# Optimization experiments

Measured on AMD Instinct MI355X. Metric: run time of the kernel, lower is better.

Reference implementation:

```python
import jax, jax.numpy as jnp
import numpy as np

N = 50000      # nodes
E = 800000     # edges
H = 128        # hidden_dim
EF = 16        # edge_feat_dim
EIN = 2 * H + 1 + EF  # edge MLP input dim = 273


def setup_inputs() -> dict:
    key = jax.random.key(0)
    ks = jax.random.split(key, 20)
    s = 0.05
    return {
        "h": jax.random.normal(ks[0], (N, H), jnp.float32),
        "x": jax.random.normal(ks[1], (N, 3), jnp.float32),
        "edge_attr": jax.random.normal(ks[2], (E, EF), jnp.float32),
        # edge MLP: Linear(EIN,H) -> SiLU -> Linear(H,H) -> SiLU
        "we_w1": jax.random.normal(ks[3], (EIN, H), jnp.float32) * s,
        "we_b1": jnp.zeros((H,), jnp.float32),
        "we_w2": jax.random.normal(ks[4], (H, H), jnp.float32) * s,
        "we_b2": jnp.zeros((H,), jnp.float32),
        # coord MLP: Linear(H,H) -> SiLU -> Linear(H,1, bias=False), tiny init
        "wc_w1": jax.random.normal(ks[5], (H, H), jnp.float32) * s,
        "wc_b1": jnp.zeros((H,), jnp.float32),
        "wc_w2": jax.random.normal(ks[6], (H, 1), jnp.float32) * 0.001,
        # node MLP: Linear(2H,H) -> SiLU -> Linear(H,H)
        "wn_w1": jax.random.normal(ks[7], (2 * H, H), jnp.float32) * s,
        "wn_b1": jnp.zeros((H,), jnp.float32),
        "wn_w2": jax.random.normal(ks[8], (H, H), jnp.float32) * s,
        "wn_b2": jnp.zeros((H,), jnp.float32),
        # layer norm
        "ln_g": jnp.ones((H,), jnp.float32),
        "ln_b": jnp.zeros((H,), jnp.float32),
        "edge_index": jax.random.randint(ks[9], (2, E), 0, N, dtype=jnp.int32),
    }


def reference(h, x, edge_attr, we_w1, we_b1, we_w2, we_b2,
              wc_w1, wc_b1, wc_w2, wn_w1, wn_b1, wn_w2, wn_b2,
              ln_g, ln_b, edge_index):
    row, col = edge_index[0], edge_index[1]
    n = h.shape[0]

    coord_diff = x[row] - x[col]                         # [E, 3]
    dist_sq = jnp.sum(coord_diff ** 2, axis=-1, keepdims=True)  # [E, 1]

    edge_input = jnp.concatenate([h[row], h[col], dist_sq, edge_attr], axis=-1)  # [E, EIN]
    m_ij = jax.nn.silu(edge_input @ we_w1 + we_b1)
    m_ij = jax.nn.silu(m_ij @ we_w2 + we_b2)             # [E, H]

    # coordinate update
    coord_w = jnp.tanh(jax.nn.silu(m_ij @ wc_w1 + wc_b1) @ wc_w2)  # [E, 1]
    dist = jnp.sqrt(dist_sq + 1e-8)
    weighted_diff = (coord_diff / dist) * coord_w        # [E, 3]
    x_update = jax.ops.segment_sum(weighted_diff, row, num_segments=n)
    degree = jax.ops.segment_sum(jnp.ones((row.shape[0], 1), x.dtype), row, num_segments=n)
    degree = jnp.maximum(degree, 1.0)
    x_out = x + x_update / degree

    # node update with residual + layernorm
    m_i = jax.ops.segment_sum(m_ij, row, num_segments=n)  # [N, H]
    node_input = jnp.concatenate([h, m_i], axis=-1)       # [N, 2H]
    h_res = h + (jax.nn.silu(node_input @ wn_w1 + wn_b1) @ wn_w2 + wn_b2)

    mu = jnp.mean(h_res, axis=-1, keepdims=True)
    var = jnp.var(h_res, axis=-1, keepdims=True)
    h_out = (h_res - mu) * jax.lax.rsqrt(var + 1e-5) * ln_g + ln_b
    return (h_out, x_out)
```

## Files before the change

kernel.cpp:

```cpp
#include <hip/hip_runtime.h>

typedef unsigned short u16;
typedef unsigned int u32;
using short8 = __attribute__((ext_vector_type(8))) short;
using f32x4  = __attribute__((ext_vector_type(4))) float;
using u32x4  = __attribute__((ext_vector_type(4))) u32;

#define N_CNT 50000
#define E_CNT 800000
#define EB_CNT 400000

__device__ __forceinline__ u16 f2bf(float f) {
  u32 u = __builtin_bit_cast(u32, f);
  u += 0x7fffu + ((u >> 16) & 1u);
  return (u16)(u >> 16);
}
__device__ __forceinline__ float bf2f(u16 v) {
  u32 u = ((u32)v) << 16;
  return __builtin_bit_cast(float, u);
}
__device__ __forceinline__ float siluf(float v) {
  return __fdividef(v, 1.f + __expf(-v));
}

__global__ void k_wf(const float* __restrict__ w1, const float* __restrict__ w2,
                     const float* __restrict__ wc1, const float* __restrict__ wn1,
                     const float* __restrict__ wn2,
                     u16* __restrict__ wef, u16* __restrict__ w1abf,
                     u16* __restrict__ wnf) {
  int idx = blockIdx.x * 256 + threadIdx.x;
  int i = idx & 7, l = (idx >> 3) & 63;
  int kb = 8 * (l >> 4) + i;
  int n16 = l & 15;
  if (idx < 4096) {
    int t = idx >> 9;
    int k = kb, n = 16 * t + n16;
    wef[idx] = (k < 17) ? f2bf(w1[(256 + k) * 128 + n]) : (u16)0;
  } else if (idx < 20480) {
    int u = idx - 4096, rest = u >> 9;
    int s = rest & 3, t = rest >> 2;
    wef[idx] = f2bf(w2[(32 * s + kb) * 128 + 16 * t + n16]);
  } else if (idx < 36864) {
    int u = idx - 20480, rest = u >> 9;
    int s = rest & 3, t = rest >> 2;
    wef[idx] = f2bf(wc1[(32 * s + kb) * 128 + 16 * t + n16]);
  } else if (idx < 69632) {
    int u = idx - 36864, rest = u >> 9;
    int s = rest & 3, t = rest >> 2;
    int k = 32 * s + kb, n = 16 * t + n16;
    float v = (n < 128) ? w1[k * 128 + n] : w1[(128 + k) * 128 + (n - 128)];
    w1abf[u] = f2bf(v);
  } else if (idx < 102400) {
    int u = idx - 69632, rest = u >> 9;
    int s = rest & 7, t = rest >> 3;
    wnf[u] = f2bf(wn1[(32 * s + kb) * 128 + 16 * t + n16]);
  } else if (idx < 118784) {
    int u = idx - 102400, rest = u >> 9;
    int s = rest & 3, t = rest >> 2;
    wnf[32768 + u] = f2bf(wn2[(32 * s + kb) * 128 + 16 * t + n16]);
  }
}

__global__ __launch_bounds__(256)
void k_hp(const float* __restrict__ h, const u16* __restrict__ w1abf,
          const float* __restrict__ b1v, u16* __restrict__ hp) {
  extern __shared__ char smem[];
  u16* wl = (u16*)smem;
  const int tid = threadIdx.x;
  {
    const u32x4* src = reinterpret_cast<const u32x4*>(w1abf);
    u32x4* dst = reinterpret_cast<u32x4*>(smem);
    for (int i2 = tid; i2 < 4096; i2 += 256) dst[i2] = src[i2];
  }
  __syncthreads();
  const int w = tid >> 6, lane = tid & 63;
  const int g = lane >> 4, c15 = lane & 15;
  float b1r[8];
#pragma unroll
  for (int t = 0; t < 8; ++t) b1r[t] = b1v[t * 16 + c15];

  int wt = blockIdx.x * 4 + w;
  if (wt >= 3125) return;
  int nbase = wt * 16;
  int nr = nbase + c15;
  short8 af[4];
#pragma unroll
  for (int s = 0; s < 4; ++s) {
    const float* p = h + nr * 128 + s * 32 + g * 8;
    f32x4 v0 = *reinterpret_cast<const f32x4*>(p);
    f32x4 v1 = *reinterpret_cast<const f32x4*>(p + 4);
    short8 t8;
#pragma unroll
    for (int j = 0; j < 4; ++j) t8[j] = (short)f2bf(v0[j]);
#pragma unroll
    for (int j = 0; j < 4; ++j) t8[4 + j] = (short)f2bf(v1[j]);
    af[s] = t8;
  }
  f32x4 acc[16];
#pragma unroll
  for (int t = 0; t < 16; ++t) acc[t] = (f32x4){0.f, 0.f, 0.f, 0.f};
#pragma unroll
  for (int s = 0; s < 4; ++s) {
#pragma unroll
    for (int t = 0; t < 16; ++t) {
      short8 bf = *reinterpret_cast<const short8*>(wl + ((t * 4 + s) * 64 + lane) * 8);
      acc[t] = __builtin_amdgcn_mfma_f32_16x16x32_bf16(af[s], bf, acc[t], 0, 0, 0);
    }
  }
#pragma unroll
  for (int t = 0; t < 16; ++t)
#pragma unroll
    for (int i = 0; i < 4; ++i) {
      int row = nbase + g * 4 + i;
      float v = acc[t][i] + ((t < 8) ? b1r[t] : 0.f);
      hp[row * 256 + t * 16 + c15] = f2bf(v);
    }
}

__global__ void k_deg(const int* __restrict__ eidx, int* __restrict__ degs) {
  int e = blockIdx.x * 256 + threadIdx.x;
  int b = (e >= EB_CNT) ? 1 : 0;
  atomicAdd(&degs[b * N_CNT + eidx[e]], 1);
}

__global__ __launch_bounds__(1024)
void k_scan2(const int* __restrict__ degs, int* __restrict__ rps) {
  const int* deg = degs + blockIdx.x * N_CNT;
  int* rp = rps + blockIdx.x * (N_CNT + 1);
  __shared__ int wsum[16];
  __shared__ int carry_s;
  int tid = threadIdx.x, lane = tid & 63, wv = tid >> 6;
  if (tid == 0) carry_s = 0;
  __syncthreads();
  for (int base = 0; base < 50176; base += 1024) {
    int idx = base + tid;
    int v = (idx < N_CNT) ? deg[idx] : 0;
    int inc = v;
#pragma unroll
    for (int d = 1; d < 64; d <<= 1) {
      int u = __shfl_up(inc, d, 64);
      if (lane >= d) inc += u;
    }
    if (lane == 63) wsum[wv] = inc;
    __syncthreads();
    if (tid < 16) {
      int s = wsum[tid];
#pragma unroll
      for (int d = 1; d < 16; d <<= 1) {
        int u = __shfl_up(s, d, 16);
        if (tid >= d) s += u;
      }
      wsum[tid] = s;
    }
    __syncthreads();
    int carry = carry_s;
    int woff = (wv > 0) ? wsum[wv - 1] : 0;
    if (idx < N_CNT) rp[idx] = carry + woff + inc - v;
    __syncthreads();
    if (tid == 0) carry_s = carry + wsum[15];
    __syncthreads();
  }
  if (threadIdx.x == 0) rp[N_CNT] = EB_CNT;
}

__global__ void k_scatter(const int* __restrict__ eidx, const int* __restrict__ rps,
                          int* __restrict__ curs, int* __restrict__ pos) {
  int e = blockIdx.x * 256 + threadIdx.x;
  int b = (e >= EB_CNT) ? 1 : 0;
  int r = eidx[e];
  int p = atomicAdd(&curs[b * N_CNT + r], 1);
  pos[e] = rps[b * (N_CNT + 1) + r] + p;
}

__global__ __launch_bounds__(1024)
void egnn_edge2(const u16* __restrict__ hp, const float* __restrict__ xc,
                const float* __restrict__ ea, const int* __restrict__ eidx,
                const int* __restrict__ pos, const u16* __restrict__ wef,
                const float* __restrict__ b2v, const float* __restrict__ bc1v,
                const float* __restrict__ wc2v,
                u16* __restrict__ m_ij, float* __restrict__ x_acc, int ebase0) {
  extern __shared__ char smem[];
  const int tid = threadIdx.x;
  {
    const u32x4* src = reinterpret_cast<const u32x4*>(wef);
    u32x4* dst = reinterpret_cast<u32x4*>(smem);
    for (int i2 = tid; i2 < 4608; i2 += 1024) dst[i2] = src[i2];
  }
  __syncthreads();
  const int w = tid >> 6, lane = tid & 63;
  const int g = lane >> 4, c15 = lane & 15;
  const int e4 = lane >> 2, q4 = lane & 3;
  const u16* w1tf = (const u16*)smem;
  const u16* w2f  = (const u16*)(smem + 8192);
  const u16* wc1f = (const u16*)(smem + 40960);
  u16* mbuf = (u16*)(smem + 73728 + w * 4352);

  float b2r[8], bc1r[8], wc2r[8];
#pragma unroll
  for (int t = 0; t < 8; ++t) {
    b2r[t]  = b2v[t * 16 + c15];
    bc1r[t] = bc1v[t * 16 + c15];
    wc2r[t] = wc2v[t * 16 + c15];
  }

  for (int bt = blockIdx.x; bt < 1563; bt += gridDim.x) {
    int wt = bt * 16 + w;
    if (wt >= 25000) continue;
    const int eb = ebase0 + wt * 16;
    int r_v = 0, c_v = 0, p_v = 0;
    if (lane < 16) {
      int gi = eb + lane;
      r_v = eidx[gi]; c_v = eidx[E_CNT + gi]; p_v = pos[gi];
      float d0 = xc[3 * r_v + 0] - xc[3 * c_v + 0];
      float d1 = xc[3 * r_v + 1] - xc[3 * c_v + 1];
      float d2 = xc[3 * r_v + 2] - xc[3 * c_v + 2];
      float dsq = d0 * d0 + d1 * d1 + d2 * d2;
      f32x4 cd = {d0, d1, d2, dsq};
      *reinterpret_cast<f32x4*>(mbuf + lane * 136 + 128) = cd;
    }
    int re4 = __shfl(r_v, e4, 64);
    int ce4 = __shfl(c_v, e4, 64);
    int pc15 = __shfl(p_v, c15, 64);
    short8 ga[4], gb[4];
    {
      const u16* pa = hp + re4 * 256 + q4 * 32;
      const u16* pb = hp + ce4 * 256 + 128 + q4 * 32;
#pragma unroll
      for (int q = 0; q < 4; ++q) ga[q] = *reinterpret_cast<const short8*>(pa + q * 8);
#pragma unroll
      for (int q = 0; q < 4; ++q) gb[q] = *reinterpret_cast<const short8*>(pb + q * 8);
    }
    {
      f32x4 eav = *reinterpret_cast<const f32x4*>(ea + (size_t)(eb + e4) * 16 + q4 * 4);
#pragma unroll
      for (int jj = 0; jj < 4; ++jj)
        mbuf[e4 * 136 + 1 + q4 * 4 + jj] = f2bf(eav[jj]);
      if (q4 == 0) {
        float dq = reinterpret_cast<const float*>(mbuf + e4 * 136 + 128)[3];
        mbuf[e4 * 136] = f2bf(dq);
      }
#pragma unroll
      for (int z = 17 + q4; z < 32; z += 4) mbuf[e4 * 136 + z] = 0;
    }
    short8 af8 = *reinterpret_cast<const short8*>(mbuf + c15 * 136 + g * 8);
    f32x4 acc[8];
#pragma unroll
    for (int t = 0; t < 8; ++t) acc[t] = (f32x4){0.f, 0.f, 0.f, 0.f};
#pragma unroll
    for (int t = 0; t < 8; ++t) {
      short8 bf = *reinterpret_cast<const short8*>(w1tf + (t * 64 + lane) * 8);
      acc[t] = __builtin_amdgcn_mfma_f32_16x16x32_bf16(af8, bf, acc[t], 0, 0, 0);
    }
#pragma unroll
    for (int t = 0; t < 8; ++t)
#pragma unroll
      for (int i = 0; i < 4; ++i)
        mbuf[(g * 4 + i) * 136 + t * 16 + c15] = f2bf(acc[t][i]);
#pragma unroll
    for (int q = 0; q < 4; ++q) {
      short8 tl = *reinterpret_cast<const short8*>(mbuf + e4 * 136 + q4 * 32 + q * 8);
      short8 o;
#pragma unroll
      for (int j = 0; j < 8; ++j) {
        float v = bf2f((u16)tl[j]) + bf2f((u16)ga[q][j]) + bf2f((u16)gb[q][j]);
        o[j] = (short)f2bf(siluf(v));
      }
      *reinterpret_cast<short8*>(mbuf + e4 * 136 + q4 * 32 + q * 8) = o;
    }
    short8 a2[4];
#pragma unroll
    for (int s = 0; s < 4; ++s)
      a2[s] = *reinterpret_cast<const short8*>(mbuf + c15 * 136 + s * 32 + g * 8);
    f32x4 acc2[8];
#pragma unroll
    for (int t = 0; t < 8; ++t) acc2[t] = (f32x4){0.f, 0.f, 0.f, 0.f};
#pragma unroll
    for (int s = 0; s < 4; ++s) {
#pragma unroll
      for (int t = 0; t < 8; ++t) {
        short8 bf = *reinterpret_cast<const short8*>(w2f + ((t * 4 + s) * 64 + lane) * 8);
        acc2[t] = __builtin_amdgcn_mfma_f32_16x16x32_bf16(a2[s], bf, acc2[t], 0, 0, 0);
      }
    }
#pragma unroll
    for (int t = 0; t < 8; ++t)
#pragma unroll
      for (int i = 0; i < 4; ++i) {
        float v = siluf(acc2[t][i] + b2r[t]);
        mbuf[(g * 4 + i) * 136 + t * 16 + c15] = f2bf(v);
      }
    short8 a3[4];
#pragma unroll
    for (int q = 0; q < 4; ++q) {
      a3[q] = *reinterpret_cast<const short8*>(mbuf + c15 * 136 + q * 32 + g * 8);
      *reinterpret_cast<short8*>(m_ij + (size_t)pc15 * 128 + q * 32 + g * 8) = a3[q];
    }
    f32x4 acc3[8];
#pragma unroll
    for (int t = 0; t < 8; ++t) acc3[t] = (f32x4){0.f, 0.f, 0.f, 0.f};
#pragma unroll
    for (int s = 0; s < 4; ++s) {
#pragma unroll
      for (int t = 0; t < 8; ++t) {
        short8 bf = *reinterpret_cast<const short8*>(wc1f + ((t * 4 + s) * 64 + lane) * 8);
        acc3[t] = __builtin_amdgcn_mfma_f32_16x16x32_bf16(a3[s], bf, acc3[t], 0, 0, 0);
      }
    }
    float p4[4] = {0.f, 0.f, 0.f, 0.f};
#pragma unroll
    for (int t = 0; t < 8; ++t)
#pragma unroll
      for (int i = 0; i < 4; ++i)
        p4[i] += siluf(acc3[t][i] + bc1r[t]) * wc2r[t];
#pragma unroll
    for (int m = 1; m <= 8; m <<= 1) {
#pragma unroll
      for (int i = 0; i < 4; ++i) p4[i] += __shfl_xor(p4[i], m, 64);
    }
    int rr[4];
#pragma unroll
    for (int i = 0; i < 4; ++i) rr[i] = __shfl(r_v, g * 4 + i, 64);
    if (c15 == 0) {
#pragma unroll
      for (int i = 0; i < 4; ++i) {
        f32x4 cd = *reinterpret_cast<const f32x4*>(mbuf + (g * 4 + i) * 136 + 128);
        float fac = rsqrtf(cd[3] + 1e-8f) * tanhf(p4[i]);
        atomicAdd(&x_acc[rr[i] * 4 + 0], cd[0] * fac);
        atomicAdd(&x_acc[rr[i] * 4 + 1], cd[1] * fac);
        atomicAdd(&x_acc[rr[i] * 4 + 2], cd[2] * fac);
      }
    }
  }
}

template <int ACC>
__global__ __launch_bounds__(256)
void k_gather(const u16* __restrict__ m_ij, const int* __restrict__ rp,
              float* __restrict__ m_i) {
  const int tid = threadIdx.x, w = tid >> 6, lane = tid & 63;
  const int grp = lane >> 4, c16 = lane & 15;
  int node = blockIdx.x * 4 + w;
  int beg = rp[node], end = rp[node + 1];
  float a[8] = {0.f, 0.f, 0.f, 0.f, 0.f, 0.f, 0.f, 0.f};
  for (int j = beg + grp; j < end; j += 4) {
    short8 v = *reinterpret_cast<const short8*>(m_ij + (size_t)j * 128 + c16 * 8);
#pragma unroll
    for (int k = 0; k < 8; ++k) a[k] += bf2f((u16)v[k]);
  }
#pragma unroll
  for (int k = 0; k < 8; ++k) {
    a[k] += __shfl_xor(a[k], 16, 64);
    a[k] += __shfl_xor(a[k], 32, 64);
  }
  if (grp == 0) {
    float* dst = m_i + node * 128 + c16 * 8;
    if (ACC) {
      f32x4 o0 = *reinterpret_cast<const f32x4*>(dst);
      f32x4 o1 = *reinterpret_cast<const f32x4*>(dst + 4);
#pragma unroll
      for (int k = 0; k < 4; ++k) { o0[k] += a[k]; o1[k] += a[4 + k]; }
      *reinterpret_cast<f32x4*>(dst) = o0;
      *reinterpret_cast<f32x4*>(dst + 4) = o1;
    } else {
      f32x4 o0 = {a[0], a[1], a[2], a[3]};
      f32x4 o1 = {a[4], a[5], a[6], a[7]};
      *reinterpret_cast<f32x4*>(dst) = o0;
      *reinterpret_cast<f32x4*>(dst + 4) = o1;
    }
  }
}

__global__ __launch_bounds__(256)
void egnn_node2(const float* __restrict__ h, const float* __restrict__ m_i,
                const u16* __restrict__ wnf,
                const float* __restrict__ bn1, const float* __restrict__ bn2,
                const float* __restrict__ lng, const float* __restrict__ lnb,
                float* __restrict__ h_out) {
  __shared__ u16 mbuf_all[4][2176];
  const int tid = threadIdx.x, w = tid >> 6, lane = tid & 63;
  const int g = lane >> 4, c15 = lane & 15;
  u16* mbuf = mbuf_all[w];
  const u16* wn1f = wnf;
  const u16* wn2f = wnf + 32768;

  float bn1r[8], bn2r[8], lngr[8], lnbr[8];
#pragma unroll
  for (int t = 0; t < 8; ++t) {
    bn1r[t] = bn1[t * 16 + c15];
    bn2r[t] = bn2[t * 16 + c15];
    lngr[t] = lng[t * 16 + c15];
    lnbr[t] = lnb[t * 16 + c15];
  }

  int wt = blockIdx.x * 4 + w;
  if (wt >= 3125) return;
  int nbase = wt * 16;
  int nr = nbase + c15;
  short8 af[8];
#pragma unroll
  for (int s = 0; s < 4; ++s) {
    const float* p = h + nr * 128 + s * 32 + g * 8;
    f32x4 v0 = *reinterpret_cast<const f32x4*>(p);
    f32x4 v1 = *reinterpret_cast<const f32x4*>(p + 4);
    short8 t8;
#pragma unroll
    for (int j = 0; j < 4; ++j) t8[j] = (short)f2bf(v0[j]);
#pragma unroll
    for (int j = 0; j < 4; ++j) t8[4 + j] = (short)f2bf(v1[j]);
    af[s] = t8;
  }
#pragma unroll
  for (int s = 0; s < 4; ++s) {
    const float* p = m_i + nr * 128 + s * 32 + g * 8;
    f32x4 v0 = *reinterpret_cast<const f32x4*>(p);
    f32x4 v1 = *reinterpret_cast<const f32x4*>(p + 4);
    short8 t8;
#pragma unroll
    for (int j = 0; j < 4; ++j) t8[j] = (short)f2bf(v0[j]);
#pragma unroll
    for (int j = 0; j < 4; ++j) t8[4 + j] = (short)f2bf(v1[j]);
    af[4 + s] = t8;
  }
  f32x4 acc[8];
#pragma unroll
  for (int t = 0; t < 8; ++t) acc[t] = (f32x4){0.f, 0.f, 0.f, 0.f};
#pragma unroll
  for (int s = 0; s < 8; ++s) {
#pragma unroll
    for (int t = 0; t < 8; ++t) {
      short8 bf = *reinterpret_cast<const short8*>(wn1f + ((t * 8 + s) * 64 + lane) * 8);
      acc[t] = __builtin_amdgcn_mfma_f32_16x16x32_bf16(af[s], bf, acc[t], 0, 0, 0);
    }
  }
#pragma unroll
  for (int t = 0; t < 8; ++t)
#pragma unroll
    for (int i = 0; i < 4; ++i) {
      float v = siluf(acc[t][i] + bn1r[t]);
      mbuf[(g * 4 + i) * 136 + t * 16 + c15] = f2bf(v);
    }
  short8 a2[4];
#pragma unroll
  for (int s = 0; s < 4; ++s)
    a2[s] = *reinterpret_cast<const short8*>(mbuf + c15 * 136 + s * 32 + g * 8);
  f32x4 acc2[8];
#pragma unroll
  for (int t = 0; t < 8; ++t) acc2[t] = (f32x4){0.f, 0.f, 0.f, 0.f};
#pragma unroll
  for (int s = 0; s < 4; ++s) {
#pragma unroll
    for (int t = 0; t < 8; ++t) {
      short8 bf = *reinterpret_cast<const short8*>(wn2f + ((t * 4 + s) * 64 + lane) * 8);
      acc2[t] = __builtin_amdgcn_mfma_f32_16x16x32_bf16(a2[s], bf, acc2[t], 0, 0, 0);
    }
  }
  float vres[8][4];
  float s1[4] = {0.f, 0.f, 0.f, 0.f}, s2[4] = {0.f, 0.f, 0.f, 0.f};
#pragma unroll
  for (int t = 0; t < 8; ++t)
#pragma unroll
    for (int i = 0; i < 4; ++i) {
      int n = nbase + g * 4 + i;
      float v = acc2[t][i] + bn2r[t] + h[n * 128 + t * 16 + c15];
      vres[t][i] = v; s1[i] += v; s2[i] += v * v;
    }
#pragma unroll
  for (int m = 1; m <= 8; m <<= 1) {
#pragma unroll
    for (int i = 0; i < 4; ++i) {
      s1[i] += __shfl_xor(s1[i], m, 64);
      s2[i] += __shfl_xor(s2[i], m, 64);
    }
  }
  float mu[4], rstd[4];
#pragma unroll
  for (int i = 0; i < 4; ++i) {
    mu[i] = s1[i] * (1.0f / 128.0f);
    float var = s2[i] * (1.0f / 128.0f) - mu[i] * mu[i];
    rstd[i] = rsqrtf(var + 1e-5f);
  }
#pragma unroll
  for (int t = 0; t < 8; ++t)
#pragma unroll
    for (int i = 0; i < 4; ++i) {
      int n = nbase + g * 4 + i;
      h_out[n * 128 + t * 16 + c15] =
          (vres[t][i] - mu[i]) * rstd[i] * lngr[t] + lnbr[t];
    }
}

__global__ void egnn_xout(const float* __restrict__ x, const float* __restrict__ x_acc,
                          const int* __restrict__ degs, float* __restrict__ xo) {
  int n = blockIdx.x * 256 + threadIdx.x;
  if (n < N_CNT) {
    float dg = fmaxf((float)(degs[n] + degs[N_CNT + n]), 1.0f);
    xo[n * 3 + 0] = x[n * 3 + 0] + x_acc[n * 4 + 0] / dg;
    xo[n * 3 + 1] = x[n * 3 + 1] + x_acc[n * 4 + 1] / dg;
    xo[n * 3 + 2] = x[n * 3 + 2] + x_acc[n * 4 + 2] / dg;
  }
}

extern "C" void kernel_launch(void* const* d_in, const int* in_sizes, int n_in,
                              void* d_out, int out_size, void* d_ws, size_t ws_size,
                              hipStream_t stream) {
  const float* h     = (const float*)d_in[0];
  const float* x     = (const float*)d_in[1];
  const float* ea    = (const float*)d_in[2];
  const float* we_w1 = (const float*)d_in[3];
  const float* we_b1 = (const float*)d_in[4];
  const float* we_w2 = (const float*)d_in[5];
  const float* we_b2 = (const float*)d_in[6];
  const float* wc_w1 = (const float*)d_in[7];
  const float* wc_b1 = (const float*)d_in[8];
  const float* wc_w2 = (const float*)d_in[9];
  const float* wn_w1 = (const float*)d_in[10];
  const float* wn_b1 = (const float*)d_in[11];
  const float* wn_w2 = (const float*)d_in[12];
  const float* wn_b2 = (const float*)d_in[13];
  const float* ln_g  = (const float*)d_in[14];
  const float* ln_b  = (const float*)d_in[15];
  const int* eidx    = (const int*)d_in[16];
  float* out = (float*)d_out;
  char* ws = (char*)d_ws;

  u16* wef    = (u16*)(ws);
  u16* w1abf  = (u16*)(ws + 73728);
  u16* wnf    = (u16*)(ws + 139264);
  u16* hp     = (u16*)(ws + 237568);
  float* m_i  = (float*)(ws + 25837568);
  float* xacc = (float*)(ws + 51437568);
  int* degs   = (int*)(ws + 52237568);
  int* curs   = (int*)(ws + 52637568);
  int* rps    = (int*)(ws + 53037568);
  int* pos    = (int*)(ws + 53437584);
  u16* m_ij   = (u16*)(ws + 56637584);

  k_wf<<<464, 256, 0, stream>>>(we_w1, we_w2, wc_w1, wn_w1, wn_w2, wef, w1abf, wnf);

  hipFuncSetAttribute(reinterpret_cast<const void*>(k_hp),
                      hipFuncAttributeMaxDynamicSharedMemorySize, 65536);
  k_hp<<<782, 256, 65536, stream>>>(h, w1abf, we_b1, hp);

  hipMemsetAsync(ws + 51437568, 0, 1600000, stream);
  k_deg<<<3125, 256, 0, stream>>>(eidx, degs);
  k_scan2<<<2, 1024, 0, stream>>>(degs, rps);
  k_scatter<<<3125, 256, 0, stream>>>(eidx, rps, curs, pos);

  hipFuncSetAttribute(reinterpret_cast<const void*>(egnn_edge2),
                      hipFuncAttributeMaxDynamicSharedMemorySize, 143360);
  egnn_edge2<<<256, 1024, 143360, stream>>>(hp, x, ea, eidx, pos, wef,
                                            we_b2, wc_b1, wc_w2, m_ij, xacc, 0);
  k_gather<0><<<12500, 256, 0, stream>>>(m_ij, rps, m_i);
  egnn_edge2<<<256, 1024, 143360, stream>>>(hp, x, ea, eidx, pos, wef,
                                            we_b2, wc_b1, wc_w2, m_ij, xacc, EB_CNT);
  k_gather<1><<<12500, 256, 0, stream>>>(m_ij, rps + (N_CNT + 1), m_i);

  egnn_node2<<<782, 256, 0, stream>>>(h, m_i, wnf, wn_b1, wn_b2, ln_g, ln_b, out);
  egnn_xout<<<196, 256, 0, stream>>>(x, xacc, degs, out + 6400000);
}
```

Measured before the change: 503.8 us.

## Parallelize row-pointer scan and retile edge kernel for higher occupancy

```diff
diff --git a/kernel.cpp b/kernel.cpp
--- a/kernel.cpp
+++ b/kernel.cpp
@@ -18,6 +18,14 @@
 __device__ __forceinline__ float bf2f(u16 v) {
   u32 u = ((u32)v) << 16;
   return __builtin_bit_cast(float, u);
+}
+__device__ __forceinline__ short8 pack8(f32x4 v0, f32x4 v1) {
+  short8 r;
+#pragma unroll
+  for (int j = 0; j < 4; ++j) r[j] = (short)f2bf(v0[j]);
+#pragma unroll
+  for (int j = 0; j < 4; ++j) r[4 + j] = (short)f2bf(v1[j]);
+  return r;
 }
 __device__ __forceinline__ float siluf(float v) {
   return __fdividef(v, 1.f + __expf(-v));
@@ -87,14 +95,8 @@
 #pragma unroll
   for (int s = 0; s < 4; ++s) {
     const float* p = h + nr * 128 + s * 32 + g * 8;
-    f32x4 v0 = *reinterpret_cast<const f32x4*>(p);
-    f32x4 v1 = *reinterpret_cast<const f32x4*>(p + 4);
-    short8 t8;
-#pragma unroll
-    for (int j = 0; j < 4; ++j) t8[j] = (short)f2bf(v0[j]);
-#pragma unroll
-    for (int j = 0; j < 4; ++j) t8[4 + j] = (short)f2bf(v1[j]);
-    af[s] = t8;
+    af[s] = pack8(*reinterpret_cast<const f32x4*>(p),
+                  *reinterpret_cast<const f32x4*>(p + 4));
   }
   f32x4 acc[16];
 #pragma unroll
@@ -108,13 +110,13 @@
     }
   }
 #pragma unroll
-  for (int t = 0; t < 16; ++t)
-#pragma unroll
-    for (int i = 0; i < 4; ++i) {
-      int row = nbase + g * 4 + i;
-      float v = acc[t][i] + ((t < 8) ? b1r[t] : 0.f);
-      hp[row * 256 + t * 16 + c15] = f2bf(v);
-    }
+  for (int t = 0; t < 16; ++t) {
+    float bb = (t < 8) ? b1r[t] : 0.f;
+    int col = t * 16 + c15;
+#pragma unroll
+    for (int i = 0; i < 4; ++i)
+      hp[(size_t)(nbase + g * 4 + i) * 256 + col] = f2bf(acc[t][i] + bb);
+  }
 }
 
 __global__ void k_deg(const int* __restrict__ eidx, int* __restrict__ degs) {
@@ -123,44 +125,67 @@
   atomicAdd(&degs[b * N_CNT + eidx[e]], 1);
 }
 
-__global__ __launch_bounds__(1024)
-void k_scan2(const int* __restrict__ degs, int* __restrict__ rps) {
-  const int* deg = degs + blockIdx.x * N_CNT;
-  int* rp = rps + blockIdx.x * (N_CNT + 1);
-  __shared__ int wsum[16];
-  __shared__ int carry_s;
-  int tid = threadIdx.x, lane = tid & 63, wv = tid >> 6;
-  if (tid == 0) carry_s = 0;
+__global__ void k_bsum(const int* __restrict__ degs, int* __restrict__ bsum) {
+  int bid = blockIdx.x;
+  int batch = bid / 98, chunk = bid % 98;
+  const int* deg = degs + batch * N_CNT;
+  int b0 = chunk * 512 + threadIdx.x;
+  int b1 = b0 + 256;
+  int v = ((b0 < N_CNT) ? deg[b0] : 0) + ((b1 < N_CNT) ? deg[b1] : 0);
+#pragma unroll
+  for (int m = 1; m <= 32; m <<= 1) v += __shfl_xor(v, m, 64);
+  __shared__ int ws[4];
+  if ((threadIdx.x & 63) == 0) ws[threadIdx.x >> 6] = v;
   __syncthreads();
-  for (int base = 0; base < 50176; base += 1024) {
-    int idx = base + tid;
-    int v = (idx < N_CNT) ? deg[idx] : 0;
+  if (threadIdx.x == 0) bsum[bid] = ws[0] + ws[1] + ws[2] + ws[3];
+}
+
+__global__ void k_mid(const int* __restrict__ bsum, int* __restrict__ boff,
+                      int* __restrict__ rps) {
+  int wv = threadIdx.x >> 6, lane = threadIdx.x & 63;
+  if (wv >= 2) return;
+  const int* bs = bsum + wv * 98;
+  int* bo = boff + wv * 98;
+  int carry = 0;
+  for (int base = 0; base < 98; base += 64) {
+    int idx = base + lane;
+    int v = (idx < 98) ? bs[idx] : 0;
     int inc = v;
 #pragma unroll
-    for (int d = 1; d < 64; d <<= 1) {
+    for (int d = 1; d <= 32; d <<= 1) {
       int u = __shfl_up(inc, d, 64);
       if (lane >= d) inc += u;
     }
-    if (lane == 63) wsum[wv] = inc;
-    __syncthreads();
-    if (tid < 16) {
-      int s = wsum[tid];
-#pragma unroll
-      for (int d = 1; d < 16; d <<= 1) {
-        int u = __shfl_up(s, d, 16);
-        if (tid >= d) s += u;
-      }
-      wsum[tid] = s;
-    }
-    __syncthreads();
-    int carry = carry_s;
-    int woff = (wv > 0) ? wsum[wv - 1] : 0;
-    if (idx < N_CNT) rp[idx] = carry + woff + inc - v;
-    __syncthreads();
-    if (tid == 0) carry_s = carry + wsum[15];
-    __syncthreads();
-  }
-  if (threadIdx.x == 0) rp[N_CNT] = EB_CNT;
+    if (idx < 98) bo[idx] = carry + inc - v;
+    carry += __shfl(inc, 63, 64);
+  }
+  if (lane == 0) rps[wv * (N_CNT + 1) + N_CNT] = EB_CNT;
+}
+
+__global__ void k_rp(const int* __restrict__ degs, const int* __restrict__ boff,
+                     int* __restrict__ rps) {
+  int bid = blockIdx.x;
+  int batch = bid / 98, chunk = bid % 98;
+  const int* deg = degs + batch * N_CNT;
+  int* rp = rps + batch * (N_CNT + 1);
+  int i0 = chunk * 512 + 2 * threadIdx.x, i1 = i0 + 1;
+  int a = (i0 < N_CNT) ? deg[i0] : 0;
+  int b = (i1 < N_CNT) ? deg[i1] : 0;
+  int s = a + b, lane = threadIdx.x & 63, wv = threadIdx.x >> 6;
+  int inc = s;
+#pragma unroll
+  for (int d = 1; d <= 32; d <<= 1) {
+    int u = __shfl_up(inc, d, 64);
+    if (lane >= d) inc += u;
+  }
+  __shared__ int ws2[4];
+  if (lane == 63) ws2[wv] = inc;
+  __syncthreads();
+  int woff = 0;
+  for (int k = 0; k < wv; ++k) woff += ws2[k];
+  int excl = boff[bid] + woff + inc - s;
+  if (i0 < N_CNT) rp[i0] = excl;
+  if (i1 < N_CNT) rp[i1] = excl + a;
 }
 
 __global__ void k_scatter(const int* __restrict__ eidx, const int* __restrict__ rps,
@@ -172,28 +197,28 @@
   pos[e] = rps[b * (N_CNT + 1) + r] + p;
 }
 
-__global__ __launch_bounds__(1024)
-void egnn_edge2(const u16* __restrict__ hp, const float* __restrict__ xc,
+__global__ __launch_bounds__(512, 4)
+void egnn_edge3(const u16* __restrict__ hp, const float* __restrict__ xc,
                 const float* __restrict__ ea, const int* __restrict__ eidx,
                 const int* __restrict__ pos, const u16* __restrict__ wef,
                 const float* __restrict__ b2v, const float* __restrict__ bc1v,
                 const float* __restrict__ wc2v,
                 u16* __restrict__ m_ij, float* __restrict__ x_acc, int ebase0) {
-  extern __shared__ char smem[];
+  __shared__ u16 w1tf[4096];
+  __shared__ u16 mbuf_all[8][2176];
   const int tid = threadIdx.x;
   {
     const u32x4* src = reinterpret_cast<const u32x4*>(wef);
-    u32x4* dst = reinterpret_cast<u32x4*>(smem);
-    for (int i2 = tid; i2 < 4608; i2 += 1024) dst[i2] = src[i2];
+    u32x4* dst = reinterpret_cast<u32x4*>(w1tf);
+    dst[tid] = src[tid];
   }
   __syncthreads();
   const int w = tid >> 6, lane = tid & 63;
   const int g = lane >> 4, c15 = lane & 15;
   const int e4 = lane >> 2, q4 = lane & 3;
-  const u16* w1tf = (const u16*)smem;
-  const u16* w2f  = (const u16*)(smem + 8192);
-  const u16* wc1f = (const u16*)(smem + 40960);
-  u16* mbuf = (u16*)(smem + 73728 + w * 4352);
+  u16* mbuf = mbuf_all[w];
+  const u16* w2g  = wef + 4096;
+  const u16* wc1g = wef + 20480;
 
   float b2r[8], bc1r[8], wc2r[8];
 #pragma unroll
@@ -203,9 +228,8 @@
     wc2r[t] = wc2v[t * 16 + c15];
   }
 
-  for (int bt = blockIdx.x; bt < 1563; bt += gridDim.x) {
-    int wt = bt * 16 + w;
-    if (wt >= 25000) continue;
+  for (int bt = blockIdx.x; bt < 3125; bt += gridDim.x) {
+    int wt = bt * 8 + w;
     const int eb = ebase0 + wt * 16;
     int r_v = 0, c_v = 0, p_v = 0;
     if (lane < 16) {
@@ -218,29 +242,30 @@
       f32x4 cd = {d0, d1, d2, dsq};
       *reinterpret_cast<f32x4*>(mbuf + lane * 136 + 128) = cd;
     }
-    int re4 = __shfl(r_v, e4, 64);
-    int ce4 = __shfl(c_v, e4, 64);
-    int pc15 = __shfl(p_v, c15, 64);
+    int re = __shfl(r_v, c15, 64);
+    int ce = __shfl(c_v, c15, 64);
+    int pc = __shfl(p_v, c15, 64);
     short8 ga[4], gb[4];
     {
-      const u16* pa = hp + re4 * 256 + q4 * 32;
-      const u16* pb = hp + ce4 * 256 + 128 + q4 * 32;
-#pragma unroll
-      for (int q = 0; q < 4; ++q) ga[q] = *reinterpret_cast<const short8*>(pa + q * 8);
-#pragma unroll
-      for (int q = 0; q < 4; ++q) gb[q] = *reinterpret_cast<const short8*>(pb + q * 8);
+      const u16* pa = hp + (size_t)re * 256 + g * 8;
+      const u16* pb = hp + (size_t)ce * 256 + 128 + g * 8;
+#pragma unroll
+      for (int s = 0; s < 4; ++s) ga[s] = *reinterpret_cast<const short8*>(pa + s * 32);
+#pragma unroll
+      for (int s = 0; s < 4; ++s) gb[s] = *reinterpret_cast<const short8*>(pb + s * 32);
     }
     {
+      u16* row = mbuf + e4 * 136;
       f32x4 eav = *reinterpret_cast<const f32x4*>(ea + (size_t)(eb + e4) * 16 + q4 * 4);
 #pragma unroll
       for (int jj = 0; jj < 4; ++jj)
-        mbuf[e4 * 136 + 1 + q4 * 4 + jj] = f2bf(eav[jj]);
+        row[1 + q4 * 4 + jj] = f2bf(eav[jj]);
       if (q4 == 0) {
-        float dq = reinterpret_cast<const float*>(mbuf + e4 * 136 + 128)[3];
-        mbuf[e4 * 136] = f2bf(dq);
+        float dq = reinterpret_cast<const float*>(row + 128)[3];
+        row[0] = f2bf(dq);
       }
 #pragma unroll
-      for (int z = 17 + q4; z < 32; z += 4) mbuf[e4 * 136 + z] = 0;
+      for (int z = 17 + q4; z < 32; z += 4) row[z] = 0;
     }
     short8 af8 = *reinterpret_cast<const short8*>(mbuf + c15 * 136 + g * 8);
     f32x4 acc[8];
@@ -252,25 +277,24 @@
       acc[t] = __builtin_amdgcn_mfma_f32_16x16x32_bf16(af8, bf, acc[t], 0, 0, 0);
     }
 #pragma unroll
-    for (int t = 0; t < 8; ++t)
+    for (int t = 0; t < 8; ++t) {
+      int col = t * 16 + c15;
 #pragma unroll
       for (int i = 0; i < 4; ++i)
-        mbuf[(g * 4 + i) * 136 + t * 16 + c15] = f2bf(acc[t][i]);
-#pragma unroll
-    for (int q = 0; q < 4; ++q) {
-      short8 tl = *reinterpret_cast<const short8*>(mbuf + e4 * 136 + q4 * 32 + q * 8);
+        mbuf[(g * 4 + i) * 136 + col] = f2bf(acc[t][i]);
+    }
+    short8 a2[4];
+#pragma unroll
+    for (int s = 0; s < 4; ++s) {
+      short8 tl = *reinterpret_cast<const short8*>(mbuf + c15 * 136 + s * 32 + g * 8);
       short8 o;
 #pragma unroll
       for (int j = 0; j < 8; ++j) {
-        float v = bf2f((u16)tl[j]) + bf2f((u16)ga[q][j]) + bf2f((u16)gb[q][j]);
+        float v = bf2f((u16)tl[j]) + bf2f((u16)ga[s][j]) + bf2f((u16)gb[s][j]);
         o[j] = (short)f2bf(siluf(v));
       }
-      *reinterpret_cast<short8*>(mbuf + e4 * 136 + q4 * 32 + q * 8) = o;
-    }
-    short8 a2[4];
-#pragma unroll
-    for (int s = 0; s < 4; ++s)
-      a2[s] = *reinterpret_cast<const short8*>(mbuf + c15 * 136 + s * 32 + g * 8);
+      a2[s] = o;
+    }
     f32x4 acc2[8];
 #pragma unroll
     for (int t = 0; t < 8; ++t) acc2[t] = (f32x4){0.f, 0.f, 0.f, 0.f};
@@ -278,22 +302,22 @@
     for (int s = 0; s < 4; ++s) {
 #pragma unroll
       for (int t = 0; t < 8; ++t) {
-        short8 bf = *reinterpret_cast<const short8*>(w2f + ((t * 4 + s) * 64 + lane) * 8);
+        short8 bf = *reinterpret_cast<const short8*>(w2g + ((t * 4 + s) * 64 + lane) * 8);
         acc2[t] = __builtin_amdgcn_mfma_f32_16x16x32_bf16(a2[s], bf, acc2[t], 0, 0, 0);
       }
     }
 #pragma unroll
-    for (int t = 0; t < 8; ++t)
-#pragma unroll
-      for (int i = 0; i < 4; ++i) {
-        float v = siluf(acc2[t][i] + b2r[t]);
-        mbuf[(g * 4 + i) * 136 + t * 16 + c15] = f2bf(v);
-      }
+    for (int t = 0; t < 8; ++t) {
+      int col = t * 16 + c15;
+#pragma unroll
+      for (int i = 0; i < 4; ++i)
+        mbuf[(g * 4 + i) * 136 + col] = f2bf(siluf(acc2[t][i] + b2r[t]));
+    }
     short8 a3[4];
 #pragma unroll
-    for (int q = 0; q < 4; ++q) {
-      a3[q] = *reinterpret_cast<const short8*>(mbuf + c15 * 136 + q * 32 + g * 8);
-      *reinterpret_cast<short8*>(m_ij + (size_t)pc15 * 128 + q * 32 + g * 8) = a3[q];
+    for (int s = 0; s < 4; ++s) {
+      a3[s] = *reinterpret_cast<const short8*>(mbuf + c15 * 136 + s * 32 + g * 8);
+      *reinterpret_cast<short8*>(m_ij + (size_t)pc * 128 + s * 32 + g * 8) = a3[s];
     }
     f32x4 acc3[8];
 #pragma unroll
@@ -302,7 +326,7 @@
     for (int s = 0; s < 4; ++s) {
 #pragma unroll
       for (int t = 0; t < 8; ++t) {
-        short8 bf = *reinterpret_cast<const short8*>(wc1f + ((t * 4 + s) * 64 + lane) * 8);
+        short8 bf = *reinterpret_cast<const short8*>(wc1g + ((t * 4 + s) * 64 + lane) * 8);
         acc3[t] = __builtin_amdgcn_mfma_f32_16x16x32_bf16(a3[s], bf, acc3[t], 0, 0, 0);
       }
     }
@@ -400,26 +424,14 @@
 #pragma unroll
   for (int s = 0; s < 4; ++s) {
     const float* p = h + nr * 128 + s * 32 + g * 8;
-    f32x4 v0 = *reinterpret_cast<const f32x4*>(p);
-    f32x4 v1 = *reinterpret_cast<const f32x4*>(p + 4);
-    short8 t8;
-#pragma unroll
-    for (int j = 0; j < 4; ++j) t8[j] = (short)f2bf(v0[j]);
-#pragma unroll
-    for (int j = 0; j < 4; ++j) t8[4 + j] = (short)f2bf(v1[j]);
-    af[s] = t8;
+    af[s] = pack8(*reinterpret_cast<const f32x4*>(p),
+                  *reinterpret_cast<const f32x4*>(p + 4));
   }
 #pragma unroll
   for (int s = 0; s < 4; ++s) {
     const float* p = m_i + nr * 128 + s * 32 + g * 8;
-    f32x4 v0 = *reinterpret_cast<const f32x4*>(p);
-    f32x4 v1 = *reinterpret_cast<const f32x4*>(p + 4);
-    short8 t8;
-#pragma unroll
-    for (int j = 0; j < 4; ++j) t8[j] = (short)f2bf(v0[j]);
-#pragma unroll
-    for (int j = 0; j < 4; ++j) t8[4 + j] = (short)f2bf(v1[j]);
-    af[4 + s] = t8;
+    af[4 + s] = pack8(*reinterpret_cast<const f32x4*>(p),
+                      *reinterpret_cast<const f32x4*>(p + 4));
   }
   f32x4 acc[8];
 #pragma unroll
@@ -433,12 +445,12 @@
     }
   }
 #pragma unroll
-  for (int t = 0; t < 8; ++t)
-#pragma unroll
-    for (int i = 0; i < 4; ++i) {
-      float v = siluf(acc[t][i] + bn1r[t]);
-      mbuf[(g * 4 + i) * 136 + t * 16 + c15] = f2bf(v);
-    }
+  for (int t = 0; t < 8; ++t) {
+    int col = t * 16 + c15;
+#pragma unroll
+    for (int i = 0; i < 4; ++i)
+      mbuf[(g * 4 + i) * 136 + col] = f2bf(siluf(acc[t][i] + bn1r[t]));
+  }
   short8 a2[4];
 #pragma unroll
   for (int s = 0; s < 4; ++s)
@@ -533,7 +545,9 @@
   int* curs   = (int*)(ws + 52637568);
   int* rps    = (int*)(ws + 53037568);
   int* pos    = (int*)(ws + 53437584);
-  u16* m_ij   = (u16*)(ws + 56637584);
+  int* bsum   = (int*)(ws + 56637584);
+  int* boff   = (int*)(ws + 56638384);
+  u16* m_ij   = (u16*)(ws + 56639200);
 
   k_wf<<<464, 256, 0, stream>>>(we_w1, we_w2, wc_w1, wn_w1, wn_w2, wef, w1abf, wnf);
 
@@ -543,16 +557,16 @@
 
   hipMemsetAsync(ws + 51437568, 0, 1600000, stream);
   k_deg<<<3125, 256, 0, stream>>>(eidx, degs);
-  k_scan2<<<2, 1024, 0, stream>>>(degs, rps);
+  k_bsum<<<196, 256, 0, stream>>>(degs, bsum);
+  k_mid<<<1, 128, 0, stream>>>(bsum, boff, rps);
+  k_rp<<<196, 256, 0, stream>>>(degs, boff, rps);
   k_scatter<<<3125, 256, 0, stream>>>(eidx, rps, curs, pos);
 
-  hipFuncSetAttribute(reinterpret_cast<const void*>(egnn_edge2),
-                      hipFuncAttributeMaxDynamicSharedMemorySize, 143360);
-  egnn_edge2<<<256, 1024, 143360, stream>>>(hp, x, ea, eidx, pos, wef,
-                                            we_b2, wc_b1, wc_w2, m_ij, xacc, 0);
+  egnn_edge3<<<768, 512, 0, stream>>>(hp, x, ea, eidx, pos, wef,
+                                      we_b2, wc_b1, wc_w2, m_ij, xacc, 0);
   k_gather<0><<<12500, 256, 0, stream>>>(m_ij, rps, m_i);
-  egnn_edge2<<<256, 1024, 143360, stream>>>(hp, x, ea, eidx, pos, wef,
-                                            we_b2, wc_b1, wc_w2, m_ij, xacc, EB_CNT);
+  egnn_edge3<<<768, 512, 0, stream>>>(hp, x, ea, eidx, pos, wef,
+                                      we_b2, wc_b1, wc_w2, m_ij, xacc, EB_CNT);
   k_gather<1><<<12500, 256, 0, stream>>>(m_ij, rps + (N_CNT + 1), m_i);
 
   egnn_node2<<<782, 256, 0, stream>>>(h, m_i, wnf, wn_b1, wn_b2, ln_g, ln_b, out);
```

Result: slower. 1.243 ms (+146.7%).
